# Optimization experiments

Hardware: AMD Instinct MI355X
Metric: run time of the kernel (lower is better)

Reference implementation:

```python
import jax, jax.numpy as jnp
import numpy as np
from jax import lax

N_IN = 512
N_OUT = 512
T = 2048
N_OBS = 256


def setup_inputs() -> dict:
    key = jax.random.key(0)
    k1, k2, k3, k4 = jax.random.split(key, 4)
    X = jax.random.normal(k1, (T, N_IN), dtype=jnp.float32)
    # W_init ~ randn / sqrt(n_input), matching the module's default init scale
    W_init = jax.random.normal(k2, (N_OUT, N_IN), dtype=jnp.float32) / np.sqrt(N_IN)
    theta = jax.random.normal(k3, (2,), dtype=jnp.float32) * 0.1
    observed_idx = jnp.sort(jax.random.randint(k4, (N_OBS,), 0, N_OUT, dtype=jnp.int32))
    return {"X": X, "W_init": W_init, "theta": theta, "observed_idx": observed_idx}


def reference(X, W_init, theta, observed_idx):
    lr = 1.0 / X.shape[1]  # module default lr = 1/n_input

    def step(W, x):
        y = jax.nn.sigmoid(W @ x)                       # [n_out]
        # parametrized Oja/Hebbian plasticity rule:
        #   dW = theta0 * y x^T + theta1 * y^2 * W
        dW = theta[0] * jnp.outer(y, x) + theta[1] * (y * y)[:, None] * W
        W_next = W + lr * dW
        m = y[observed_idx]                             # observed subset
        return W_next, m

    _, m_traj = lax.scan(step, W_init, X)               # m_traj: [T, n_obs]
    return m_traj
```

## Files before the change

### kernel.cpp

```cpp
#include <hip/hip_runtime.h>


constexpr int N_IN    = 512;
constexpr int T       = 2048;
constexpr int N_OBS   = 256;
constexpr int D       = 8;
constexpr int NBLK    = T / D;
constexpr int BANDPAD = 64;

typedef float f4 __attribute__((ext_vector_type(4)));

__device__ constexpr int BOFF[8] = {0, 7, 13, 18, 22, 25, 27, 28};

#define DPP_ADD(v, ctrl, rmask)                                                \
    v += __int_as_float(__builtin_amdgcn_update_dpp(                           \
        0, __float_as_int(v), (ctrl), (rmask), 0xf, false))

__device__ __forceinline__ float wave64_sum_bcast(float v) {
    DPP_ADD(v, 0x111, 0xf);
    DPP_ADD(v, 0x112, 0xf);
    DPP_ADD(v, 0x114, 0xf);
    DPP_ADD(v, 0x118, 0xf);
    DPP_ADD(v, 0x142, 0xa);
    DPP_ADD(v, 0x143, 0xc);
    return __int_as_float(__builtin_amdgcn_readlane(__float_as_int(v), 63));
}

__device__ __forceinline__ float dot8(const f4& u0, const f4& u1,
                                      const f4& v0, const f4& v1) {
    float p0 = fmaf(u0.x, v0.x, u0.y * v0.y);
    float p1 = fmaf(u0.z, v0.z, u0.w * v0.w);
    float p2 = fmaf(u1.x, v1.x, u1.y * v1.y);
    float p3 = fmaf(u1.z, v1.z, u1.w * v1.w);
    return (p0 + p1) + (p2 + p3);
}

#define GLOADX(dst, addr, offstr)                                              \
    asm volatile("global_load_dwordx4 %0, %1, off offset:" offstr              \
                 : "=v"(dst) : "v"(addr))

__device__ __forceinline__ void stage16(f4 (&xb)[16], const char* xa) {
    const char* a0 = xa;
    const char* a1 = xa + 4096;
    const char* a2 = xa + 8192;
    const char* a3 = xa + 12288;
    GLOADX(xb[0],  a0, "0");    GLOADX(xb[1],  a0, "1024");
    GLOADX(xb[2],  a0, "2048"); GLOADX(xb[3],  a0, "3072");
    GLOADX(xb[4],  a1, "0");    GLOADX(xb[5],  a1, "1024");
    GLOADX(xb[6],  a1, "2048"); GLOADX(xb[7],  a1, "3072");
    GLOADX(xb[8],  a2, "0");    GLOADX(xb[9],  a2, "1024");
    GLOADX(xb[10], a2, "2048"); GLOADX(xb[11], a2, "3072");
    GLOADX(xb[12], a3, "0");    GLOADX(xb[13], a3, "1024");
    GLOADX(xb[14], a3, "2048"); GLOADX(xb[15], a3, "3072");
}

#define TIEBUF(ins, buf)                                                       \
    asm volatile(ins                                                           \
        : "+v"(buf[0]), "+v"(buf[1]), "+v"(buf[2]),  "+v"(buf[3]),             \
          "+v"(buf[4]), "+v"(buf[5]), "+v"(buf[6]),  "+v"(buf[7]),             \
          "+v"(buf[8]), "+v"(buf[9]), "+v"(buf[10]), "+v"(buf[11]),            \
          "+v"(buf[12]),"+v"(buf[13]),"+v"(buf[14]), "+v"(buf[15]))

#define PIN(buf)      TIEBUF("", buf)
#define WAIT1(buf)    TIEBUF("s_waitcnt vmcnt(1)", buf)
#define WAIT0(buf)    TIEBUF("s_waitcnt vmcnt(0)", buf)

__global__ __launch_bounds__(64) void gram_kernel(const float* __restrict__ X,
                                                  float* __restrict__ P) {
    const int b    = blockIdx.x;
    const int lane = threadIdx.x;
    const int t0   = b * D;
    const f4* Xv = (const f4*)(X + (long)t0 * N_IN);
    f4 r[8][2];
    #pragma unroll
    for (int i = 0; i < 8; ++i) {
        r[i][0] = Xv[i * (N_IN / 4) + lane * 2 + 0];
        r[i][1] = Xv[i * (N_IN / 4) + lane * 2 + 1];
    }
    float s[28];
    #pragma unroll
    for (int i = 0; i < 7; ++i) {
        #pragma unroll
        for (int j = 1; j <= 7 - i; ++j) {
            s[BOFF[i] + j - 1] =
                wave64_sum_bcast(dot8(r[i][0], r[i][1], r[i + j][0], r[i + j][1]));
        }
    }
    if (lane == 0) {
        #pragma unroll
        for (int k = 0; k < 28; ++k) P[b * BANDPAD + k] = s[k];
    }
}

__device__ __forceinline__ void process_block(
    const f4 (&xb)[16], const float (&bs)[28], int t0, int lane, int wave,
    f4& w0, f4& w1, float th0, float th1, float* __restrict__ out)
{
    float q[D];
    #pragma unroll
    for (int d = 0; d < D; ++d)
        q[d] = wave64_sum_bcast(dot8(w0, w1, xb[2 * d], xb[2 * d + 1]));

    float ys = 0.0f;
    float z = q[0];
    #pragma unroll
    for (int i = 0; i < D; ++i) {
        const float y = __builtin_amdgcn_rcpf(1.0f + __expf(-z));
        if (lane == i) ys = y;

        const float a = th0 * y;
        const float b = fmaf(th1 * y, y, 1.0f);

        #pragma unroll
        for (int d = i + 1; d < D; ++d)
            q[d] = fmaf(b, q[d], a * bs[BOFF[i] + (d - i) - 1]);
        if (i < D - 1) z = q[i + 1];

        w0.x = fmaf(b, w0.x, a * xb[2 * i].x);
        w0.y = fmaf(b, w0.y, a * xb[2 * i].y);
        w0.z = fmaf(b, w0.z, a * xb[2 * i].z);
        w0.w = fmaf(b, w0.w, a * xb[2 * i].w);
        w1.x = fmaf(b, w1.x, a * xb[2 * i + 1].x);
        w1.y = fmaf(b, w1.y, a * xb[2 * i + 1].y);
        w1.z = fmaf(b, w1.z, a * xb[2 * i + 1].z);
        w1.w = fmaf(b, w1.w, a * xb[2 * i + 1].w);
    }

    float* oaddr = out + (size_t)(t0 + lane) * N_OBS + wave;
    asm volatile("s_mov_b64 vcc, exec\n\t"
                 "s_mov_b64 exec, 0xff\n\t"
                 "global_store_dword %0, %1, off\n\t"
                 "s_mov_b64 exec, vcc"
                 :: "v"(oaddr), "v"(ys) : "vcc");
}

__device__ __forceinline__ void load_band(float (&bs)[28], const float* pb) {
    #pragma unroll
    for (int k = 0; k < 28; ++k) bs[k] = pb[k];
}

__global__ __launch_bounds__(256, 1) void oja_scan_kernel(
    const float* __restrict__ X,
    const float* __restrict__ Winit,
    const float* __restrict__ theta,
    const int*   __restrict__ obs,
    const float* __restrict__ P,
    float*       __restrict__ out)
{
    const int tid  = threadIdx.x;
    const int wid  = tid >> 6;
    const int lane = tid & 63;
    const int wave = blockIdx.x * 4 + wid;

    const int row = obs[wave];
    const float lr  = 1.0f / (float)N_IN;
    const float th0 = theta[0] * lr;
    const float th1 = theta[1] * lr;

    const f4* Wv = (const f4*)(Winit + (long)row * N_IN);
    f4 w0 = Wv[lane];
    f4 w1 = Wv[64 + lane];

    const char* xbase = (const char*)X + (size_t)lane * 16;

    f4 xA[16], xB[16];
    float bsA[28], bsB[28];

    stage16(xA, xbase);
    load_band(bsA, P);
    WAIT0(xA);

    for (int blk = 0; blk < NBLK; blk += 2) {
        const int b1 = (blk + 1 < NBLK) ? (blk + 1) : (NBLK - 1);
        stage16(xB, xbase + (size_t)b1 * 16384);
        load_band(bsB, P + (size_t)b1 * BANDPAD);
        PIN(xA);
        process_block(xA, bsA, blk * D, lane, wave, w0, w1, th0, th1, out);
        WAIT1(xB);

        const int b2 = (blk + 2 < NBLK) ? (blk + 2) : (NBLK - 1);
        stage16(xA, xbase + (size_t)b2 * 16384);
        load_band(bsA, P + (size_t)b2 * BANDPAD);
        PIN(xB);
        process_block(xB, bsB, (blk + 1) * D, lane, wave, w0, w1, th0, th1, out);
        WAIT1(xA);
    }
}

extern "C" void kernel_launch(void* const* d_in, const int* in_sizes, int n_in,
                              void* d_out, int out_size, void* d_ws, size_t ws_size,
                              hipStream_t stream) {
    const float* X     = (const float*)d_in[0];
    const float* Winit = (const float*)d_in[1];
    const float* theta = (const float*)d_in[2];
    const int*   obs   = (const int*)d_in[3];
    float*       out   = (float*)d_out;
    float*       P     = (float*)d_ws;

    gram_kernel<<<NBLK, 64, 0, stream>>>(X, P);

    oja_scan_kernel<<<64, 256, 0, stream>>>(X, Winit, theta, obs, P, out);
}
```

Measured before the change: 291.9 us.

## Defer W updates per block via suffix-product coefficients and fold log2e scaling

The per-step rank-1 W update inside the serial 8-step chain is replaced by a single accumulated update after the chain, using coefficients built from suffix products of the per-step scale factors b. W and theta0 are pre-scaled by log2(e) so the sigmoid can call exp2 directly instead of exp. The dot products become sequential fma chains. This shortens the latency-critical dependency chain per block, at the cost of slightly different rounding and a longer serial fma chain per lane in the dot products.

```diff
diff --git a/kernel.cpp b/kernel.cpp
--- a/kernel.cpp
+++ b/kernel.cpp
@@ -7,6 +7,7 @@
 constexpr int D       = 8;
 constexpr int NBLK    = T / D;
 constexpr int BANDPAD = 64;
+constexpr float LOG2E = 1.44269504088896f;
 
 typedef float f4 __attribute__((ext_vector_type(4)));
 
@@ -26,13 +27,17 @@
     return __int_as_float(__builtin_amdgcn_readlane(__float_as_int(v), 63));
 }
 
-__device__ __forceinline__ float dot8(const f4& u0, const f4& u1,
-                                      const f4& v0, const f4& v1) {
-    float p0 = fmaf(u0.x, v0.x, u0.y * v0.y);
-    float p1 = fmaf(u0.z, v0.z, u0.w * v0.w);
-    float p2 = fmaf(u1.x, v1.x, u1.y * v1.y);
-    float p3 = fmaf(u1.z, v1.z, u1.w * v1.w);
-    return (p0 + p1) + (p2 + p3);
+__device__ __forceinline__ float dot8s(const f4& w0, const f4& w1,
+                                       const f4& x0, const f4& x1) {
+    float p = w0.x * x0.x;
+    p = fmaf(w0.y, x0.y, p);
+    p = fmaf(w0.z, x0.z, p);
+    p = fmaf(w0.w, x0.w, p);
+    p = fmaf(w1.x, x1.x, p);
+    p = fmaf(w1.y, x1.y, p);
+    p = fmaf(w1.z, x1.z, p);
+    p = fmaf(w1.w, x1.w, p);
+    return p;
 }
 
 #define GLOADX(dst, addr, offstr)                                              \
@@ -83,7 +88,7 @@
         #pragma unroll
         for (int j = 1; j <= 7 - i; ++j) {
             s[BOFF[i] + j - 1] =
-                wave64_sum_bcast(dot8(r[i][0], r[i][1], r[i + j][0], r[i + j][1]));
+                wave64_sum_bcast(dot8s(r[i][0], r[i][1], r[i + j][0], r[i + j][1]));
         }
     }
     if (lane == 0) {
@@ -94,37 +99,66 @@
 
 __device__ __forceinline__ void process_block(
     const f4 (&xb)[16], const float (&bs)[28], int t0, int lane, int wave,
-    f4& w0, f4& w1, float th0, float th1, float* __restrict__ out)
+    f4& w0, f4& w1, float th0s, float th1, float* __restrict__ out)
 {
     float q[D];
     #pragma unroll
     for (int d = 0; d < D; ++d)
-        q[d] = wave64_sum_bcast(dot8(w0, w1, xb[2 * d], xb[2 * d + 1]));
-
+        q[d] = wave64_sum_bcast(dot8s(w0, w1, xb[2 * d], xb[2 * d + 1]));
+
+    float av[D], bv[D];
     float ys = 0.0f;
     float z = q[0];
     #pragma unroll
     for (int i = 0; i < D; ++i) {
-        const float y = __builtin_amdgcn_rcpf(1.0f + __expf(-z));
+        const float y =
+            __builtin_amdgcn_rcpf(1.0f + __builtin_amdgcn_exp2f(-z));
         if (lane == i) ys = y;
 
-        const float a = th0 * y;
+        const float a = th0s * y;
         const float b = fmaf(th1 * y, y, 1.0f);
+        av[i] = a;
+        bv[i] = b;
 
         #pragma unroll
         for (int d = i + 1; d < D; ++d)
             q[d] = fmaf(b, q[d], a * bs[BOFF[i] + (d - i) - 1]);
         if (i < D - 1) z = q[i + 1];
-
-        w0.x = fmaf(b, w0.x, a * xb[2 * i].x);
-        w0.y = fmaf(b, w0.y, a * xb[2 * i].y);
-        w0.z = fmaf(b, w0.z, a * xb[2 * i].z);
-        w0.w = fmaf(b, w0.w, a * xb[2 * i].w);
-        w1.x = fmaf(b, w1.x, a * xb[2 * i + 1].x);
-        w1.y = fmaf(b, w1.y, a * xb[2 * i + 1].y);
-        w1.z = fmaf(b, w1.z, a * xb[2 * i + 1].z);
-        w1.w = fmaf(b, w1.w, a * xb[2 * i + 1].w);
-    }
+    }
+
+    float c[D];
+    float sfx = 1.0f;
+    #pragma unroll
+    for (int i = D - 1; i >= 0; --i) {
+        c[i] = av[i] * sfx;
+        sfx *= bv[i];
+    }
+    const float B = sfx;
+
+    f4 acc0, acc1;
+    acc0.x = c[0] * xb[0].x;  acc0.y = c[0] * xb[0].y;
+    acc0.z = c[0] * xb[0].z;  acc0.w = c[0] * xb[0].w;
+    acc1.x = c[0] * xb[1].x;  acc1.y = c[0] * xb[1].y;
+    acc1.z = c[0] * xb[1].z;  acc1.w = c[0] * xb[1].w;
+    #pragma unroll
+    for (int i = 1; i < D; ++i) {
+        acc0.x = fmaf(c[i], xb[2 * i].x, acc0.x);
+        acc0.y = fmaf(c[i], xb[2 * i].y, acc0.y);
+        acc0.z = fmaf(c[i], xb[2 * i].z, acc0.z);
+        acc0.w = fmaf(c[i], xb[2 * i].w, acc0.w);
+        acc1.x = fmaf(c[i], xb[2 * i + 1].x, acc1.x);
+        acc1.y = fmaf(c[i], xb[2 * i + 1].y, acc1.y);
+        acc1.z = fmaf(c[i], xb[2 * i + 1].z, acc1.z);
+        acc1.w = fmaf(c[i], xb[2 * i + 1].w, acc1.w);
+    }
+    w0.x = fmaf(B, w0.x, acc0.x);
+    w0.y = fmaf(B, w0.y, acc0.y);
+    w0.z = fmaf(B, w0.z, acc0.z);
+    w0.w = fmaf(B, w0.w, acc0.w);
+    w1.x = fmaf(B, w1.x, acc1.x);
+    w1.y = fmaf(B, w1.y, acc1.y);
+    w1.z = fmaf(B, w1.z, acc1.z);
+    w1.w = fmaf(B, w1.w, acc1.w);
 
     float* oaddr = out + (size_t)(t0 + lane) * N_OBS + wave;
     asm volatile("s_mov_b64 vcc, exec\n\t"
@@ -153,13 +187,15 @@
     const int wave = blockIdx.x * 4 + wid;
 
     const int row = obs[wave];
-    const float lr  = 1.0f / (float)N_IN;
-    const float th0 = theta[0] * lr;
-    const float th1 = theta[1] * lr;
+    const float lr   = 1.0f / (float)N_IN;
+    const float th0s = theta[0] * lr * LOG2E;
+    const float th1  = theta[1] * lr;
 
     const f4* Wv = (const f4*)(Winit + (long)row * N_IN);
     f4 w0 = Wv[lane];
     f4 w1 = Wv[64 + lane];
+    w0.x *= LOG2E; w0.y *= LOG2E; w0.z *= LOG2E; w0.w *= LOG2E;
+    w1.x *= LOG2E; w1.y *= LOG2E; w1.z *= LOG2E; w1.w *= LOG2E;
 
     const char* xbase = (const char*)X + (size_t)lane * 16;
 
@@ -175,14 +211,14 @@
         stage16(xB, xbase + (size_t)b1 * 16384);
         load_band(bsB, P + (size_t)b1 * BANDPAD);
         PIN(xA);
-        process_block(xA, bsA, blk * D, lane, wave, w0, w1, th0, th1, out);
+        process_block(xA, bsA, blk * D, lane, wave, w0, w1, th0s, th1, out);
         WAIT1(xB);
 
         const int b2 = (blk + 2 < NBLK) ? (blk + 2) : (NBLK - 1);
         stage16(xA, xbase + (size_t)b2 * 16384);
         load_band(bsA, P + (size_t)b2 * BANDPAD);
         PIN(xB);
-        process_block(xB, bsB, (blk + 1) * D, lane, wave, w0, w1, th0, th1, out);
+        process_block(xB, bsB, (blk + 1) * D, lane, wave, w0, w1, th0s, th1, out);
         WAIT1(xA);
     }
 }
```

New measurement: 249.1 us (median of 2 runs). -14.7%, faster.
